# Kernel optimization log

Measured on AMD Instinct MI355X. Metric: run time of the kernel, lower is better.

## Reference

```python
import jax, jax.numpy as jnp
import numpy as np
import math

D_HEAD = 64
EPS = 1e-6


def _rms_norm(x, scale, eps):
    # compute in float32 like the torch reference (promote_types with float32)
    xf = x.astype(jnp.float32)
    ms = jnp.mean(xf * xf, axis=-1, keepdims=True)
    return (xf * (scale.astype(jnp.float32) * jax.lax.rsqrt(ms + eps))).astype(x.dtype)


def _apply_rotary(x, cos, sin):
    # rotate first 2*cos_dim channels, pass the rest through
    ro = cos.shape[-1] * 2
    xr, xp = x[..., :ro], x[..., ro:]
    c = jnp.concatenate([cos, cos], axis=-1)
    s = jnp.concatenate([sin, sin], axis=-1)
    x1, x2 = jnp.split(xr, 2, axis=-1)
    rot = jnp.concatenate([-x2, x1], axis=-1)
    return jnp.concatenate([xr * c + rot * s, xp], axis=-1)


def _nb_idx(L, k):
    # NATTEN neighborhood start: window of size k clamped inside [0, L)
    i = jnp.arange(L)
    start = jnp.clip(i - k // 2, 0, L - k)
    return start[:, None] + jnp.arange(k)[None, :]  # [L, k]


def setup_inputs() -> dict:
    key = jax.random.key(0)
    ks = jax.random.split(key, 6)
    n, H, W, d_model, cond_features = 2, 48, 48, 256, 256
    x = jax.random.normal(ks[0], (n, H, W, d_model), dtype=jnp.float32)
    axis = jnp.linspace(-1.0, 1.0, H, dtype=jnp.float32)
    gh, gw = jnp.meshgrid(axis, axis, indexing='ij')
    pos = jnp.stack([gh, gw], axis=-1)  # [H, W, 2]
    cond = jax.random.normal(ks[1], (n, cond_features), dtype=jnp.float32)
    w_norm = jax.random.normal(ks[2], (d_model, cond_features), dtype=jnp.float32) * 0.01
    w_qkv = jax.random.normal(ks[3], (3 * d_model, d_model), dtype=jnp.float32) / math.sqrt(d_model)
    w_out = jax.random.normal(ks[4], (d_model, d_model), dtype=jnp.float32) * 0.02
    return {"x": x, "pos": pos, "cond": cond, "w_norm": w_norm, "w_qkv": w_qkv,
            "w_out": w_out, "kernel_size": 7}


def reference(x, pos, cond, w_norm, w_qkv, w_out, kernel_size):
    n, H, W, d_model = x.shape
    e = D_HEAD
    nh = d_model // e
    k = kernel_size
    skip = x

    # AdaRMSNorm: scale = linear(cond) + 1, broadcast over h, w
    scale = (cond @ w_norm.T)[:, None, None, :] + 1.0  # [n,1,1,d_model]
    xn = _rms_norm(x, scale, EPS)

    # QKV projection -> [3, n, nh, H, W, e]
    qkv = (xn @ w_qkv.T).reshape(n, H, W, 3, nh, e)
    qkv = jnp.transpose(qkv, (3, 0, 4, 1, 2, 5))
    q, kk, v = qkv[0], qkv[1], qkv[2]

    # Axial RoPE: freqs buffer of AxialRoPE(d_head // 2)
    dim = e // 2
    nf = dim // 4
    freqs = jnp.exp(jnp.linspace(math.log(math.pi), math.log(10.0 * math.pi), nf + 1)[:-1]).astype(jnp.float32)
    fh = pos[..., 0:1] * freqs  # [H,W,nf]
    fw = pos[..., 1:2] * freqs
    fr = jnp.concatenate([fh, fw], axis=-1)  # [H,W,2*nf] == [H,W,e//4]
    cos, sin = jnp.cos(fr), jnp.sin(fr)
    q = _apply_rotary(q, cos, sin)
    kk = _apply_rotary(kk, cos, sin)
    q = q / math.sqrt(e)

    # 2D neighborhood attention (natten2dqk / natten2dav, dilation 1)
    idx_h = _nb_idx(H, k)  # [H,k]
    idx_w = _nb_idx(W, k)  # [W,k]
    kg = kk[:, :, idx_h][:, :, :, :, idx_w]  # [n,nh,H,k,W,k,e]
    vg = v[:, :, idx_h][:, :, :, :, idx_w]   # [n,nh,H,k,W,k,e]
    qk = jnp.einsum('bmije,bmipjqe->bmijpq', q, kg).reshape(n, nh, H, W, k * k)
    a = jax.nn.softmax(qk, axis=-1).reshape(n, nh, H, W, k, k)
    o = jnp.einsum('bmijpq,bmipjqe->bmije', a, vg)  # [n,nh,H,W,e]

    o = jnp.transpose(o, (0, 2, 3, 1, 4)).reshape(n, H, W, d_model)
    return o @ w_out.T + skip
```

## Files before the change

### kernel.cpp

```cpp
#include <hip/hip_runtime.h>
#include <math.h>

#define N_B 2
#define HH 48
#define WW 48
#define DM 256
#define NH 4
#define EH 64
#define KS 7
#define NPIX (N_B*HH*WW)

typedef _Float16 half8 __attribute__((ext_vector_type(8)));
typedef float float4v __attribute__((ext_vector_type(4)));

__global__ void scale_kernel(const float* __restrict__ cond,
                             const float* __restrict__ w_norm,
                             float* __restrict__ scale) {
    int b = blockIdx.x;
    int t = threadIdx.x, wave = t >> 6, lane = t & 63;
    int d = blockIdx.y*32 + wave*8 + (lane >> 3);
    int l8 = lane & 7;
    const float4* wr4 = (const float4*)(w_norm + (size_t)d*DM) + l8*8;
    const float4* c4  = (const float4*)(cond + (size_t)b*DM) + l8*8;
    float acc = 0.f;
    #pragma unroll
    for (int j = 0; j < 8; ++j) {
        float4 w = wr4[j], c = c4[j];
        acc += w.x*c.x + w.y*c.y + w.z*c.z + w.w*c.w;
    }
    acc += __shfl_xor(acc, 1, 64);
    acc += __shfl_xor(acc, 2, 64);
    acc += __shfl_xor(acc, 4, 64);
    if (l8 == 0) scale[b*DM + d] = acc + 1.0f;
}

__global__ void rmsnorm_kernel(const float* __restrict__ x,
                               const float* __restrict__ scale,
                               _Float16* __restrict__ xn) {
    int pix = blockIdx.x, t = threadIdx.x;
    int b = pix / (HH*WW);
    float v = x[(size_t)pix*DM + t];
    float ss = v*v;
    #pragma unroll
    for (int off = 32; off > 0; off >>= 1) ss += __shfl_xor(ss, off, 64);
    __shared__ float wsum[4];
    if ((t & 63) == 0) wsum[t>>6] = ss;
    __syncthreads();
    float tot = wsum[0]+wsum[1]+wsum[2]+wsum[3];
    float r = rsqrtf(tot*(1.0f/DM) + 1e-6f);
    xn[(size_t)pix*DM + t] = (_Float16)(v * scale[b*DM + t] * r);
}

__global__ __launch_bounds__(256) void gemm_qkv_f16(const _Float16* __restrict__ A,
                                                    const float* __restrict__ B,
                                                    const float* __restrict__ pos,
                                                    _Float16* __restrict__ qh,
                                                    _Float16* __restrict__ kh,
                                                    _Float16* __restrict__ vh) {
    const int K = DM, LDT = 40;
    __shared__ _Float16 As[64*LDT];
    __shared__ _Float16 Bs[64*LDT];
    int t = threadIdx.x;
    int wave = t >> 6, lane = t & 63;
    int m0 = blockIdx.x*64, n0 = blockIdx.y*64;
    int lr = t >> 2, lk = (t & 3) * 8;

    float4v acc[4];
    #pragma unroll
    for (int ni = 0; ni < 4; ++ni) acc[ni] = (float4v){0.f,0.f,0.f,0.f};

    int frow = lane & 15, kq = (lane >> 4) * 8;

    for (int k0 = 0; k0 < K; k0 += 32) {
        half8 a0 = *(const half8*)(A + (size_t)(m0 + lr)*K + k0 + lk);
        const float* bp = B + (size_t)(n0 + lr)*K + k0 + lk;
        float4 b0 = *(const float4*)bp;
        float4 b1 = *(const float4*)(bp + 4);
        half8 hb;
        hb[0]=(_Float16)b0.x; hb[1]=(_Float16)b0.y; hb[2]=(_Float16)b0.z; hb[3]=(_Float16)b0.w;
        hb[4]=(_Float16)b1.x; hb[5]=(_Float16)b1.y; hb[6]=(_Float16)b1.z; hb[7]=(_Float16)b1.w;
        __syncthreads();
        *(half8*)&As[lr*LDT + lk] = a0;
        *(half8*)&Bs[lr*LDT + lk] = hb;
        __syncthreads();
        half8 af = *(const half8*)&As[(wave*16 + frow)*LDT + kq];
        #pragma unroll
        for (int ni = 0; ni < 4; ++ni) {
            half8 bf = *(const half8*)&Bs[(ni*16 + frow)*LDT + kq];
            acc[ni] = __builtin_amdgcn_mfma_f32_16x16x32_f16(af, bf, acc[ni], 0, 0, 0);
        }
    }

    int sel  = n0 >> 8;
    int head = (n0 >> 6) & 3;
    _Float16* outp = (sel == 0) ? qh : (sel == 1) ? kh : vh;
    int col = lane & 15, rbase = (lane >> 4) * 4;
    float freq = __expf(1.14472988585f + (float)(col & 7) * 0.287823136624f);
    #pragma unroll
    for (int r = 0; r < 4; ++r) {
        int pix = m0 + wave*16 + rbase + r;
        float v0 = acc[0][r], v1 = acc[1][r], v2 = acc[2][r], v3 = acc[3][r];
        if (sel < 2) {
            int hw = pix % (HH*WW);
            float p = (col < 8) ? pos[hw*2] : pos[hw*2+1];
            float sn, cs;
            __sincosf(p*freq, &sn, &cs);
            float o0 = v0*cs - v1*sn;
            float o1 = v1*cs + v0*sn;
            v0 = o0; v1 = o1;
            if (sel == 0) { v0*=0.125f; v1*=0.125f; v2*=0.125f; v3*=0.125f; }
        }
        size_t base = (size_t)pix*DM + head*EH;
        outp[base +  0 + col] = (_Float16)v0;
        outp[base + 16 + col] = (_Float16)v1;
        outp[base + 32 + col] = (_Float16)v2;
        outp[base + 48 + col] = (_Float16)v3;
    }
}

__global__ __launch_bounds__(256) void attn_mfma(const _Float16* __restrict__ qg,
                                                 const _Float16* __restrict__ kg,
                                                 const _Float16* __restrict__ vg,
                                                 _Float16* __restrict__ obuf) {
    __shared__ _Float16 VT[64*232];
    __shared__ _Float16 SP[64*232];
    int t = threadIdx.x;
    int wave = t >> 6, lane = t & 63;
    int col = lane & 15, quad = lane >> 4;
    int ty = blockIdx.x / 6, tx = blockIdx.x % 6;
    int b = blockIdx.y >> 2, head = blockIdx.y & 3;
    int qh0 = ty*8, qw0 = tx*8;
    int rh0 = min(max(qh0-3, 0), HH-14);
    int rw0 = min(max(qw0-3, 0), WW-14);

    {
        int nbl = t & 31;
        int e0  = (t >> 5) * 8;
        #pragma unroll
        for (int pass = 0; pass < 7; ++pass) {
            int nb = pass*32 + nbl;
            int nr = nb >> 4, nc = nb & 15;
            int pix = (b*HH + rh0+nr)*WW + rw0 + nc;
            half8 vv = *(const half8*)(vg + (size_t)pix*DM + head*EH + e0);
            #pragma unroll
            for (int i = 0; i < 8; ++i)
                VT[(e0+i)*232 + nb] = vv[i];
        }
    }

    int qidx_a = wave*16 + col;
    int pixq = (b*HH + qh0 + (qidx_a>>3))*WW + qw0 + (qidx_a & 7);
    const _Float16* qp = qg + (size_t)pixq*DM + head*EH;
    half8 qf0 = *(const half8*)(qp + quad*8);
    half8 qf1 = *(const half8*)(qp + 32 + quad*8);

    float4v s[14];
    #pragma unroll
    for (int nr = 0; nr < 14; ++nr) {
        int pixk = (b*HH + rh0+nr)*WW + rw0 + col;
        const _Float16* kp = kg + (size_t)pixk*DM + head*EH;
        half8 kf0 = *(const half8*)(kp + quad*8);
        half8 kf1 = *(const half8*)(kp + 32 + quad*8);
        float4v a = (float4v){0.f,0.f,0.f,0.f};
        a = __builtin_amdgcn_mfma_f32_16x16x32_f16(qf0, kf0, a, 0, 0, 0);
        a = __builtin_amdgcn_mfma_f32_16x16x32_f16(qf1, kf1, a, 0, 0, 0);
        s[nr] = a;
    }

    int sh_[4], uw_[4];
    #pragma unroll
    for (int r = 0; r < 4; ++r) {
        int qidx = wave*16 + quad*4 + r;
        int qhh = qh0 + (qidx>>3), qww = qw0 + (qidx & 7);
        sh_[r] = min(max(qhh-3, 0), HH-KS);
        int sw_ = min(max(qww-3, 0), WW-KS);
        uw_[r] = rw0 + col - sw_;
    }
    #pragma unroll
    for (int nr = 0; nr < 14; ++nr)
        #pragma unroll
        for (int r = 0; r < 4; ++r) {
            int uh = rh0 + nr - sh_[r];
            bool ok = ((unsigned)uh < 7u) && ((unsigned)uw_[r] < 7u);
            s[nr][r] = ok ? s[nr][r] : -1e30f;
        }
    #pragma unroll
    for (int r = 0; r < 4; ++r) {
        float m = s[0][r];
        #pragma unroll
        for (int nr = 1; nr < 14; ++nr) m = fmaxf(m, s[nr][r]);
        m = fmaxf(m, __shfl_xor(m, 1, 64));
        m = fmaxf(m, __shfl_xor(m, 2, 64));
        m = fmaxf(m, __shfl_xor(m, 4, 64));
        m = fmaxf(m, __shfl_xor(m, 8, 64));
        float sum = 0.f;
        #pragma unroll
        for (int nr = 0; nr < 14; ++nr) { float p = __expf(s[nr][r] - m); s[nr][r] = p; sum += p; }
        sum += __shfl_xor(sum, 1, 64);
        sum += __shfl_xor(sum, 2, 64);
        sum += __shfl_xor(sum, 4, 64);
        sum += __shfl_xor(sum, 8, 64);
        float rs = 1.f / sum;
        #pragma unroll
        for (int nr = 0; nr < 14; ++nr)
            SP[(wave*16 + quad*4 + r)*232 + nr*16 + col] = (_Float16)(s[nr][r] * rs);
    }
    __syncthreads();

    float4v o[4];
    #pragma unroll
    for (int dt = 0; dt < 4; ++dt) o[dt] = (float4v){0.f,0.f,0.f,0.f};
    #pragma unroll
    for (int ks = 0; ks < 7; ++ks) {
        half8 pa = *(const half8*)&SP[(wave*16 + col)*232 + ks*32 + quad*8];
        #pragma unroll
        for (int dt = 0; dt < 4; ++dt) {
            half8 vf = *(const half8*)&VT[(dt*16 + col)*232 + ks*32 + quad*8];
            o[dt] = __builtin_amdgcn_mfma_f32_16x16x32_f16(pa, vf, o[dt], 0, 0, 0);
        }
    }
    #pragma unroll
    for (int r = 0; r < 4; ++r) {
        int qidx = wave*16 + quad*4 + r;
        int pix = (b*HH + qh0 + (qidx>>3))*WW + qw0 + (qidx & 7);
        #pragma unroll
        for (int dt = 0; dt < 4; ++dt)
            obuf[(size_t)pix*DM + head*EH + dt*16 + col] = (_Float16)o[dt][r];
    }
}

__global__ __launch_bounds__(256) void gemm_out_f16(const _Float16* __restrict__ A,
                                                    const float* __restrict__ B,
                                                    float* __restrict__ C,
                                                    const float* __restrict__ skip) {
    const int K = DM, N = DM, LDT = 40;
    __shared__ _Float16 As[64*LDT];
    __shared__ _Float16 Bs[64*LDT];
    int t = threadIdx.x;
    int wave = t >> 6, lane = t & 63;
    int m0 = blockIdx.x*64, n0 = blockIdx.y*64;
    int lr = t >> 2, lk = (t & 3) * 8;

    float4v acc[4];
    #pragma unroll
    for (int ni = 0; ni < 4; ++ni) acc[ni] = (float4v){0.f,0.f,0.f,0.f};

    int frow = lane & 15, kq = (lane >> 4) * 8;

    for (int k0 = 0; k0 < K; k0 += 32) {
        half8 a0 = *(const half8*)(A + (size_t)(m0 + lr)*K + k0 + lk);
        const float* bp = B + (size_t)(n0 + lr)*K + k0 + lk;
        float4 b0 = *(const float4*)bp;
        float4 b1 = *(const float4*)(bp + 4);
        half8 hb;
        hb[0]=(_Float16)b0.x; hb[1]=(_Float16)b0.y; hb[2]=(_Float16)b0.z; hb[3]=(_Float16)b0.w;
        hb[4]=(_Float16)b1.x; hb[5]=(_Float16)b1.y; hb[6]=(_Float16)b1.z; hb[7]=(_Float16)b1.w;
        __syncthreads();
        *(half8*)&As[lr*LDT + lk] = a0;
        *(half8*)&Bs[lr*LDT + lk] = hb;
        __syncthreads();
        half8 af = *(const half8*)&As[(wave*16 + frow)*LDT + kq];
        #pragma unroll
        for (int ni = 0; ni < 4; ++ni) {
            half8 bf = *(const half8*)&Bs[(ni*16 + frow)*LDT + kq];
            acc[ni] = __builtin_amdgcn_mfma_f32_16x16x32_f16(af, bf, acc[ni], 0, 0, 0);
        }
    }

    int col = lane & 15, rbase = (lane >> 4) * 4;
    #pragma unroll
    for (int ni = 0; ni < 4; ++ni) {
        #pragma unroll
        for (int r = 0; r < 4; ++r) {
            int row = m0 + wave*16 + rbase + r;
            int c   = n0 + ni*16 + col;
            C[(size_t)row*N + c] = acc[ni][r] + skip[(size_t)row*N + c];
        }
    }
}

extern "C" void kernel_launch(void* const* d_in, const int* in_sizes, int n_in,
                              void* d_out, int out_size, void* d_ws, size_t ws_size,
                              hipStream_t stream) {
    const float* x      = (const float*)d_in[0];
    const float* pos    = (const float*)d_in[1];
    const float* cond   = (const float*)d_in[2];
    const float* w_norm = (const float*)d_in[3];
    const float* w_qkv  = (const float*)d_in[4];
    const float* w_out  = (const float*)d_in[5];
    float* out = (float*)d_out;
    char* base = (char*)d_ws;

    const size_t SZH = (size_t)NPIX*DM*2;
    const size_t PAD = 4096;
    float*    scale  = (float*)(base);
    _Float16* xn_h   = (_Float16*)(base + PAD);
    _Float16* qh     = (_Float16*)(base + PAD + 1*(SZH+PAD));
    _Float16* kh     = (_Float16*)(base + PAD + 2*(SZH+PAD));
    _Float16* vh     = (_Float16*)(base + PAD + 3*(SZH+PAD));
    _Float16* obuf_h = (_Float16*)(base + PAD + 4*(SZH+PAD));

    scale_kernel<<<dim3(N_B, 8), 256, 0, stream>>>(cond, w_norm, scale);
    rmsnorm_kernel<<<dim3(NPIX), dim3(DM), 0, stream>>>(x, scale, xn_h);
    gemm_qkv_f16<<<dim3(NPIX/64, 12), 256, 0, stream>>>(xn_h, w_qkv, pos, qh, kh, vh);
    attn_mfma<<<dim3(36, N_B*NH), 256, 0, stream>>>(qh, kh, vh, obuf_h);
    gemm_out_f16<<<dim3(NPIX/64, DM/64), 256, 0, stream>>>(obuf_h, w_out, out, x);
}
```

Baseline: 105.3 us.

## Fuse RMSNorm into QKV GEMM and double-buffer weight tiles in both GEMMs

Removes the separate rmsnorm kernel. The QKV GEMM now normalizes each 64-row x tile straight into shared memory as fp16, which drops a global round trip of the normalized activations and one launch. Both GEMMs keep the full-K A tile resident in LDS and double-buffer the fp32-to-fp16 weight tiles with register prefetch, so there is one barrier per K step instead of two. The QKV GEMM also widens its N tile to 128 and gives each wave a 2x4 MFMA tile, which means fewer blocks and more LDS per block. Each QKV block now recomputes the norm for its rows, so every x row is read and normalized six times.

```diff
diff --git a/kernel.cpp b/kernel.cpp
--- a/kernel.cpp
+++ b/kernel.cpp
@@ -11,6 +11,7 @@
 #define NPIX (N_B*HH*WW)
 
 typedef _Float16 half8 __attribute__((ext_vector_type(8)));
+typedef _Float16 half4v __attribute__((ext_vector_type(4)));
 typedef float float4v __attribute__((ext_vector_type(4)));
 
 __global__ void scale_kernel(const float* __restrict__ cond,
@@ -34,87 +35,128 @@
     if (l8 == 0) scale[b*DM + d] = acc + 1.0f;
 }
 
-__global__ void rmsnorm_kernel(const float* __restrict__ x,
-                               const float* __restrict__ scale,
-                               _Float16* __restrict__ xn) {
-    int pix = blockIdx.x, t = threadIdx.x;
-    int b = pix / (HH*WW);
-    float v = x[(size_t)pix*DM + t];
-    float ss = v*v;
-    #pragma unroll
-    for (int off = 32; off > 0; off >>= 1) ss += __shfl_xor(ss, off, 64);
-    __shared__ float wsum[4];
-    if ((t & 63) == 0) wsum[t>>6] = ss;
-    __syncthreads();
-    float tot = wsum[0]+wsum[1]+wsum[2]+wsum[3];
-    float r = rsqrtf(tot*(1.0f/DM) + 1e-6f);
-    xn[(size_t)pix*DM + t] = (_Float16)(v * scale[b*DM + t] * r);
-}
-
-__global__ __launch_bounds__(256) void gemm_qkv_f16(const _Float16* __restrict__ A,
-                                                    const float* __restrict__ B,
-                                                    const float* __restrict__ pos,
-                                                    _Float16* __restrict__ qh,
-                                                    _Float16* __restrict__ kh,
-                                                    _Float16* __restrict__ vh) {
-    const int K = DM, LDT = 40;
-    __shared__ _Float16 As[64*LDT];
-    __shared__ _Float16 Bs[64*LDT];
+__global__ __launch_bounds__(256) void gemm_qkv_fused(const float* __restrict__ x,
+                                                      const float* __restrict__ scale,
+                                                      const float* __restrict__ B,
+                                                      const float* __restrict__ pos,
+                                                      _Float16* __restrict__ qh,
+                                                      _Float16* __restrict__ kh,
+                                                      _Float16* __restrict__ vh) {
+    const int LDA = 264, LDB = 40;
+    __shared__ _Float16 As[64*LDA];
+    __shared__ _Float16 Bs[2][128*LDB];
     int t = threadIdx.x;
     int wave = t >> 6, lane = t & 63;
-    int m0 = blockIdx.x*64, n0 = blockIdx.y*64;
-    int lr = t >> 2, lk = (t & 3) * 8;
-
-    float4v acc[4];
-    #pragma unroll
-    for (int ni = 0; ni < 4; ++ni) acc[ni] = (float4v){0.f,0.f,0.f,0.f};
-
-    int frow = lane & 15, kq = (lane >> 4) * 8;
-
-    for (int k0 = 0; k0 < K; k0 += 32) {
-        half8 a0 = *(const half8*)(A + (size_t)(m0 + lr)*K + k0 + lk);
-        const float* bp = B + (size_t)(n0 + lr)*K + k0 + lk;
-        float4 b0 = *(const float4*)bp;
-        float4 b1 = *(const float4*)(bp + 4);
-        half8 hb;
-        hb[0]=(_Float16)b0.x; hb[1]=(_Float16)b0.y; hb[2]=(_Float16)b0.z; hb[3]=(_Float16)b0.w;
-        hb[4]=(_Float16)b1.x; hb[5]=(_Float16)b1.y; hb[6]=(_Float16)b1.z; hb[7]=(_Float16)b1.w;
-        __syncthreads();
-        *(half8*)&As[lr*LDT + lk] = a0;
-        *(half8*)&Bs[lr*LDT + lk] = hb;
-        __syncthreads();
-        half8 af = *(const half8*)&As[(wave*16 + frow)*LDT + kq];
+    int m0 = blockIdx.x*64;
+    int n0 = blockIdx.y*128;
+    int b  = m0 / (HH*WW);
+
+    {
+        int tr = t >> 2, c4 = t & 3;
+        const float4* xr = (const float4*)(x + (size_t)(m0 + tr)*DM);
+        float4 xv[16];
+        float ss = 0.f;
+        #pragma unroll
+        for (int j = 0; j < 16; ++j) {
+            xv[j] = xr[c4 + j*4];
+            ss += xv[j].x*xv[j].x + xv[j].y*xv[j].y + xv[j].z*xv[j].z + xv[j].w*xv[j].w;
+        }
+        ss += __shfl_xor(ss, 1, 64);
+        ss += __shfl_xor(ss, 2, 64);
+        float r = rsqrtf(ss*(1.0f/DM) + 1e-6f);
+        const float* sc = scale + b*DM;
+        #pragma unroll
+        for (int j = 0; j < 16; ++j) {
+            int c = (c4 + j*4)*4;
+            float4 s4 = *(const float4*)(sc + c);
+            half4v h;
+            h[0] = (_Float16)(xv[j].x * s4.x * r);
+            h[1] = (_Float16)(xv[j].y * s4.y * r);
+            h[2] = (_Float16)(xv[j].z * s4.z * r);
+            h[3] = (_Float16)(xv[j].w * s4.w * r);
+            *(half4v*)&As[tr*LDA + c] = h;
+        }
+    }
+    int br = t >> 1, kk = (t & 1)*16;
+    {
+        const float* bp = B + (size_t)(n0 + br)*DM + kk;
+        float4 b0 = ((const float4*)bp)[0], b1 = ((const float4*)bp)[1];
+        float4 b2 = ((const float4*)bp)[2], b3 = ((const float4*)bp)[3];
+        half8 h0, h1;
+        h0[0]=(_Float16)b0.x; h0[1]=(_Float16)b0.y; h0[2]=(_Float16)b0.z; h0[3]=(_Float16)b0.w;
+        h0[4]=(_Float16)b1.x; h0[5]=(_Float16)b1.y; h0[6]=(_Float16)b1.z; h0[7]=(_Float16)b1.w;
+        h1[0]=(_Float16)b2.x; h1[1]=(_Float16)b2.y; h1[2]=(_Float16)b2.z; h1[3]=(_Float16)b2.w;
+        h1[4]=(_Float16)b3.x; h1[5]=(_Float16)b3.y; h1[6]=(_Float16)b3.z; h1[7]=(_Float16)b3.w;
+        *(half8*)&Bs[0][br*LDB + kk]     = h0;
+        *(half8*)&Bs[0][br*LDB + kk + 8] = h1;
+    }
+    __syncthreads();
+
+    float4v acc[2][4];
+    #pragma unroll
+    for (int mi = 0; mi < 2; ++mi)
+        #pragma unroll
+        for (int ni = 0; ni < 4; ++ni) acc[mi][ni] = (float4v){0.f,0.f,0.f,0.f};
+
+    int frow = lane & 15, kq = (lane >> 4)*8;
+    int wm = wave >> 1, wn = wave & 1;
+
+    for (int it = 0; it < 8; ++it) {
+        int cur = it & 1;
+        float4 nb0, nb1, nb2, nb3;
+        if (it < 7) {
+            const float* bp = B + (size_t)(n0 + br)*DM + (it + 1)*32 + kk;
+            nb0 = ((const float4*)bp)[0]; nb1 = ((const float4*)bp)[1];
+            nb2 = ((const float4*)bp)[2]; nb3 = ((const float4*)bp)[3];
+        }
+        int ka = it*32 + kq;
+        half8 af0 = *(const half8*)&As[(wm*32 +  0 + frow)*LDA + ka];
+        half8 af1 = *(const half8*)&As[(wm*32 + 16 + frow)*LDA + ka];
         #pragma unroll
         for (int ni = 0; ni < 4; ++ni) {
-            half8 bf = *(const half8*)&Bs[(ni*16 + frow)*LDT + kq];
-            acc[ni] = __builtin_amdgcn_mfma_f32_16x16x32_f16(af, bf, acc[ni], 0, 0, 0);
-        }
-    }
-
-    int sel  = n0 >> 8;
-    int head = (n0 >> 6) & 3;
+            half8 bf = *(const half8*)&Bs[cur][(wn*64 + ni*16 + frow)*LDB + kq];
+            acc[0][ni] = __builtin_amdgcn_mfma_f32_16x16x32_f16(af0, bf, acc[0][ni], 0, 0, 0);
+            acc[1][ni] = __builtin_amdgcn_mfma_f32_16x16x32_f16(af1, bf, acc[1][ni], 0, 0, 0);
+        }
+        if (it < 7) {
+            half8 h0, h1;
+            h0[0]=(_Float16)nb0.x; h0[1]=(_Float16)nb0.y; h0[2]=(_Float16)nb0.z; h0[3]=(_Float16)nb0.w;
+            h0[4]=(_Float16)nb1.x; h0[5]=(_Float16)nb1.y; h0[6]=(_Float16)nb1.z; h0[7]=(_Float16)nb1.w;
+            h1[0]=(_Float16)nb2.x; h1[1]=(_Float16)nb2.y; h1[2]=(_Float16)nb2.z; h1[3]=(_Float16)nb2.w;
+            h1[4]=(_Float16)nb3.x; h1[5]=(_Float16)nb3.y; h1[6]=(_Float16)nb3.z; h1[7]=(_Float16)nb3.w;
+            *(half8*)&Bs[cur^1][br*LDB + kk]     = h0;
+            *(half8*)&Bs[cur^1][br*LDB + kk + 8] = h1;
+            __syncthreads();
+        }
+    }
+
+    int sel  = blockIdx.y >> 1;
+    int head = (blockIdx.y & 1)*2 + wn;
     _Float16* outp = (sel == 0) ? qh : (sel == 1) ? kh : vh;
-    int col = lane & 15, rbase = (lane >> 4) * 4;
+    int col = lane & 15, rbase = (lane >> 4)*4;
     float freq = __expf(1.14472988585f + (float)(col & 7) * 0.287823136624f);
     #pragma unroll
-    for (int r = 0; r < 4; ++r) {
-        int pix = m0 + wave*16 + rbase + r;
-        float v0 = acc[0][r], v1 = acc[1][r], v2 = acc[2][r], v3 = acc[3][r];
-        if (sel < 2) {
-            int hw = pix % (HH*WW);
-            float p = (col < 8) ? pos[hw*2] : pos[hw*2+1];
-            float sn, cs;
-            __sincosf(p*freq, &sn, &cs);
-            float o0 = v0*cs - v1*sn;
-            float o1 = v1*cs + v0*sn;
-            v0 = o0; v1 = o1;
-            if (sel == 0) { v0*=0.125f; v1*=0.125f; v2*=0.125f; v3*=0.125f; }
-        }
-        size_t base = (size_t)pix*DM + head*EH;
-        outp[base +  0 + col] = (_Float16)v0;
-        outp[base + 16 + col] = (_Float16)v1;
-        outp[base + 32 + col] = (_Float16)v2;
-        outp[base + 48 + col] = (_Float16)v3;
+    for (int mi = 0; mi < 2; ++mi) {
+        #pragma unroll
+        for (int r = 0; r < 4; ++r) {
+            int pix = m0 + wm*32 + mi*16 + rbase + r;
+            float v0 = acc[mi][0][r], v1 = acc[mi][1][r], v2 = acc[mi][2][r], v3 = acc[mi][3][r];
+            if (sel < 2) {
+                int hw = pix % (HH*WW);
+                float p = (col < 8) ? pos[hw*2] : pos[hw*2+1];
+                float sn, cs;
+                __sincosf(p*freq, &sn, &cs);
+                float o0 = v0*cs - v1*sn;
+                float o1 = v1*cs + v0*sn;
+                v0 = o0; v1 = o1;
+                if (sel == 0) { v0*=0.125f; v1*=0.125f; v2*=0.125f; v3*=0.125f; }
+            }
+            size_t base = (size_t)pix*DM + head*EH;
+            outp[base +  0 + col] = (_Float16)v0;
+            outp[base + 16 + col] = (_Float16)v1;
+            outp[base + 32 + col] = (_Float16)v2;
+            outp[base + 48 + col] = (_Float16)v3;
+        }
     }
 }
 
@@ -233,48 +275,76 @@
                                                     const float* __restrict__ B,
                                                     float* __restrict__ C,
                                                     const float* __restrict__ skip) {
-    const int K = DM, N = DM, LDT = 40;
-    __shared__ _Float16 As[64*LDT];
-    __shared__ _Float16 Bs[64*LDT];
+    const int LDA = 264, LDB = 40;
+    __shared__ _Float16 As[64*LDA];
+    __shared__ _Float16 Bs[2][64*LDB];
     int t = threadIdx.x;
     int wave = t >> 6, lane = t & 63;
     int m0 = blockIdx.x*64, n0 = blockIdx.y*64;
-    int lr = t >> 2, lk = (t & 3) * 8;
-
-    float4v acc[4];
-    #pragma unroll
-    for (int ni = 0; ni < 4; ++ni) acc[ni] = (float4v){0.f,0.f,0.f,0.f};
-
-    int frow = lane & 15, kq = (lane >> 4) * 8;
-
-    for (int k0 = 0; k0 < K; k0 += 32) {
-        half8 a0 = *(const half8*)(A + (size_t)(m0 + lr)*K + k0 + lk);
-        const float* bp = B + (size_t)(n0 + lr)*K + k0 + lk;
-        float4 b0 = *(const float4*)bp;
-        float4 b1 = *(const float4*)(bp + 4);
-        half8 hb;
-        hb[0]=(_Float16)b0.x; hb[1]=(_Float16)b0.y; hb[2]=(_Float16)b0.z; hb[3]=(_Float16)b0.w;
-        hb[4]=(_Float16)b1.x; hb[5]=(_Float16)b1.y; hb[6]=(_Float16)b1.z; hb[7]=(_Float16)b1.w;
-        __syncthreads();
-        *(half8*)&As[lr*LDT + lk] = a0;
-        *(half8*)&Bs[lr*LDT + lk] = hb;
-        __syncthreads();
-        half8 af = *(const half8*)&As[(wave*16 + frow)*LDT + kq];
-        #pragma unroll
-        for (int ni = 0; ni < 4; ++ni) {
-            half8 bf = *(const half8*)&Bs[(ni*16 + frow)*LDT + kq];
-            acc[ni] = __builtin_amdgcn_mfma_f32_16x16x32_f16(af, bf, acc[ni], 0, 0, 0);
-        }
-    }
-
-    int col = lane & 15, rbase = (lane >> 4) * 4;
-    #pragma unroll
-    for (int ni = 0; ni < 4; ++ni) {
-        #pragma unroll
-        for (int r = 0; r < 4; ++r) {
-            int row = m0 + wave*16 + rbase + r;
-            int c   = n0 + ni*16 + col;
-            C[(size_t)row*N + c] = acc[ni][r] + skip[(size_t)row*N + c];
+
+    {
+        int tr = t >> 2, c8 = (t & 3)*8;
+        const _Float16* ap = A + (size_t)(m0 + tr)*DM;
+        #pragma unroll
+        for (int j = 0; j < 8; ++j)
+            *(half8*)&As[tr*LDA + c8 + j*32] = *(const half8*)(ap + c8 + j*32);
+    }
+    int br = t >> 2, kk = (t & 3)*8;
+    {
+        const float* bp = B + (size_t)(n0 + br)*DM + kk;
+        float4 b0 = ((const float4*)bp)[0], b1 = ((const float4*)bp)[1];
+        half8 h;
+        h[0]=(_Float16)b0.x; h[1]=(_Float16)b0.y; h[2]=(_Float16)b0.z; h[3]=(_Float16)b0.w;
+        h[4]=(_Float16)b1.x; h[5]=(_Float16)b1.y; h[6]=(_Float16)b1.z; h[7]=(_Float16)b1.w;
+        *(half8*)&Bs[0][br*LDB + kk] = h;
+    }
+    __syncthreads();
+
+    float4v acc[2][2];
+    #pragma unroll
+    for (int mi = 0; mi < 2; ++mi)
+        #pragma unroll
+        for (int ni = 0; ni < 2; ++ni) acc[mi][ni] = (float4v){0.f,0.f,0.f,0.f};
+
+    int frow = lane & 15, kq = (lane >> 4)*8;
+    int wm = wave >> 1, wn = wave & 1;
+
+    for (int it = 0; it < 8; ++it) {
+        int cur = it & 1;
+        float4 nb0, nb1;
+        if (it < 7) {
+            const float* bp = B + (size_t)(n0 + br)*DM + (it + 1)*32 + kk;
+            nb0 = ((const float4*)bp)[0]; nb1 = ((const float4*)bp)[1];
+        }
+        int ka = it*32 + kq;
+        half8 af0 = *(const half8*)&As[(wm*32 +  0 + frow)*LDA + ka];
+        half8 af1 = *(const half8*)&As[(wm*32 + 16 + frow)*LDA + ka];
+        #pragma unroll
+        for (int ni = 0; ni < 2; ++ni) {
+            half8 bf = *(const half8*)&Bs[cur][(wn*32 + ni*16 + frow)*LDB + kq];
+            acc[0][ni] = __builtin_amdgcn_mfma_f32_16x16x32_f16(af0, bf, acc[0][ni], 0, 0, 0);
+            acc[1][ni] = __builtin_amdgcn_mfma_f32_16x16x32_f16(af1, bf, acc[1][ni], 0, 0, 0);
+        }
+        if (it < 7) {
+            half8 h;
+            h[0]=(_Float16)nb0.x; h[1]=(_Float16)nb0.y; h[2]=(_Float16)nb0.z; h[3]=(_Float16)nb0.w;
+            h[4]=(_Float16)nb1.x; h[5]=(_Float16)nb1.y; h[6]=(_Float16)nb1.z; h[7]=(_Float16)nb1.w;
+            *(half8*)&Bs[cur^1][br*LDB + kk] = h;
+            __syncthreads();
+        }
+    }
+
+    int col = lane & 15, rbase = (lane >> 4)*4;
+    #pragma unroll
+    for (int mi = 0; mi < 2; ++mi) {
+        #pragma unroll
+        for (int ni = 0; ni < 2; ++ni) {
+            #pragma unroll
+            for (int r = 0; r < 4; ++r) {
+                int row = m0 + wm*32 + mi*16 + rbase + r;
+                int c   = n0 + wn*32 + ni*16 + col;
+                C[(size_t)row*DM + c] = acc[mi][ni][r] + skip[(size_t)row*DM + c];
+            }
         }
     }
 }
@@ -294,15 +364,13 @@
     const size_t SZH = (size_t)NPIX*DM*2;
     const size_t PAD = 4096;
     float*    scale  = (float*)(base);
-    _Float16* xn_h   = (_Float16*)(base + PAD);
-    _Float16* qh     = (_Float16*)(base + PAD + 1*(SZH+PAD));
-    _Float16* kh     = (_Float16*)(base + PAD + 2*(SZH+PAD));
-    _Float16* vh     = (_Float16*)(base + PAD + 3*(SZH+PAD));
-    _Float16* obuf_h = (_Float16*)(base + PAD + 4*(SZH+PAD));
+    _Float16* qh     = (_Float16*)(base + PAD);
+    _Float16* kh     = (_Float16*)(base + PAD + 1*(SZH+PAD));
+    _Float16* vh     = (_Float16*)(base + PAD + 2*(SZH+PAD));
+    _Float16* obuf_h = (_Float16*)(base + PAD + 3*(SZH+PAD));
 
     scale_kernel<<<dim3(N_B, 8), 256, 0, stream>>>(cond, w_norm, scale);
-    rmsnorm_kernel<<<dim3(NPIX), dim3(DM), 0, stream>>>(x, scale, xn_h);
-    gemm_qkv_f16<<<dim3(NPIX/64, 12), 256, 0, stream>>>(xn_h, w_qkv, pos, qh, kh, vh);
+    gemm_qkv_fused<<<dim3(NPIX/64, 6), 256, 0, stream>>>(x, scale, w_qkv, pos, qh, kh, vh);
     attn_mfma<<<dim3(36, N_B*NH), 256, 0, stream>>>(qh, kh, vh, obuf_h);
     gemm_out_f16<<<dim3(NPIX/64, DM/64), 256, 0, stream>>>(obuf_h, w_out, out, x);
 }
```

Result: no change. 105.8 us (+0.4%).
